# Kernel tuning notes

Measured on AMD Instinct MI355X. Metric: run time of the kernel, lower is better.

The kernel has to match this reference:

```python
import jax, jax.numpy as jnp
import numpy as np

D_MODEL = 1024
N_HEAD = 16
DH = D_MODEL // N_HEAD


def setup_inputs() -> dict:
    key = jax.random.key(0)
    ks = jax.random.split(key, 5)
    B, T = 4, 2048
    scale = 0.02
    return {
        "x": jax.random.normal(ks[0], (B, T, D_MODEL), dtype=jnp.float32),
        "Wqkv": jax.random.normal(ks[1], (D_MODEL, 3 * D_MODEL), dtype=jnp.float32) * scale,
        "bqkv": jnp.zeros((3 * D_MODEL,), dtype=jnp.float32),
        "Wout": jax.random.normal(ks[2], (D_MODEL, D_MODEL), dtype=jnp.float32) * scale,
        "bout": jnp.zeros((D_MODEL,), dtype=jnp.float32),
    }


def reference(x, Wqkv, bqkv, Wout, bout):
    B, T, C = x.shape
    qkv = x @ Wqkv + bqkv  # [B,T,3C]
    q, k, v = jnp.split(qkv, 3, axis=2)
    # [B,T,C] -> [B,H,T,dh]
    def heads(t):
        return t.reshape(B, T, N_HEAD, DH).transpose(0, 2, 1, 3)
    q, k, v = heads(q), heads(k), heads(v)
    scores = jnp.einsum("bhqd,bhkd->bhqk", q, k) / jnp.sqrt(jnp.float32(DH))
    causal = jnp.tril(jnp.ones((T, T), dtype=bool))  # [T,T]
    neg = jnp.finfo(scores.dtype).min
    scores = jnp.where(causal[None, None, :, :], scores, neg)
    A = jax.nn.softmax(scores, axis=-1)
    y = jnp.einsum("bhqk,bhkd->bhqd", A, v)
    y = y.transpose(0, 2, 1, 3).reshape(B, T, C)
    return y @ Wout + bout
```

## Files before the change

kernel.cpp:

```cpp
#include <hip/hip_runtime.h>
#include <hip/hip_bf16.h>

typedef float f32x4 __attribute__((ext_vector_type(4)));
typedef short s16x8 __attribute__((ext_vector_type(8)));
typedef short s16x4 __attribute__((ext_vector_type(4)));

#define B_ 4
#define T_ 2048
#define C_ 1024
#define H_ 16
#define DH_ 64
#define M_ (B_*T_)
#define N3_ (3*C_)

static __device__ __forceinline__ short f2bf(float f) {
    __hip_bfloat16 h = __float2bfloat16(f);
    return *reinterpret_cast<short*>(&h);
}

static __device__ __forceinline__ void gload16(const void* g, void* l) {
    __builtin_amdgcn_global_load_lds(
        (const __attribute__((address_space(1))) void*)g,
        (__attribute__((address_space(3))) void*)l, 16, 0, 0);
}

static __device__ __forceinline__ s16x8 lds_frag(const short* base, int row, int chunk) {
    return *(const s16x8*)&base[(row << 6) + ((chunk ^ (row & 7)) << 3)];
}


__global__ __launch_bounds__(256) void cast_f32_bf16(
    const float* __restrict__ in, short* __restrict__ out, int n8)
{
    int i = blockIdx.x * 256 + threadIdx.x;
    if (i >= n8) return;
    float4 a = *(const float4*)&in[i * 8];
    float4 b = *(const float4*)&in[i * 8 + 4];
    s16x8 o = { f2bf(a.x), f2bf(a.y), f2bf(a.z), f2bf(a.w),
                f2bf(b.x), f2bf(b.y), f2bf(b.z), f2bf(b.w) };
    *(s16x8*)&out[i * 8] = o;
}

__global__ __launch_bounds__(256) void transpose_cast(
    const float* __restrict__ src, short* __restrict__ dst, int K, int N)
{
    __shared__ short t[64][66];
    int tid = threadIdx.x;
    int n0 = blockIdx.x * 64, k0 = blockIdx.y * 64;
    #pragma unroll
    for (int p = 0; p < 4; ++p) {
        int cid = tid + p * 256;
        int r = cid >> 4, c4 = cid & 15;
        float4 v = *(const float4*)&src[(size_t)(k0 + r) * N + n0 + c4 * 4];
        t[r][c4 * 4 + 0] = f2bf(v.x);
        t[r][c4 * 4 + 1] = f2bf(v.y);
        t[r][c4 * 4 + 2] = f2bf(v.z);
        t[r][c4 * 4 + 3] = f2bf(v.w);
    }
    __syncthreads();
    #pragma unroll
    for (int p = 0; p < 4; ++p) {
        int cid = tid + p * 256;
        int r = cid >> 4, c4 = cid & 15;
        s16x4 ov;
        #pragma unroll
        for (int j = 0; j < 4; ++j) ov[j] = t[c4 * 4 + j][r];
        *(s16x4*)&dst[(size_t)(n0 + r) * K + k0 + c4 * 4] = ov;
    }
}


template<int MODE>
__global__ __launch_bounds__(256) void gemm_bt(
    const short* __restrict__ A, const short* __restrict__ Bt,
    const float* __restrict__ bias, float* __restrict__ out,
    short* __restrict__ qout, short* __restrict__ kout, short* __restrict__ vout)
{
    const int K = 1024;
    __shared__ short As[128 * 64];
    __shared__ short Bs[128 * 64];
    int tid = threadIdx.x;
    int lane = tid & 63, w = tid >> 6;
    int d = lane & 15, g = lane >> 4;
    int wm = w >> 1, wn = w & 1;
    int m0 = blockIdx.y * 128, n0 = blockIdx.x * 128;

    f32x4 acc[4][4];
    #pragma unroll
    for (int i = 0; i < 4; ++i)
        #pragma unroll
        for (int j = 0; j < 4; ++j) acc[i][j] = (f32x4){0.f, 0.f, 0.f, 0.f};

    for (int kt = 0; kt < K; kt += 64) {
        #pragma unroll
        for (int p = 0; p < 4; ++p) {
            int cid = p * 256 + tid;
            int r = cid >> 3, c8 = cid & 7;
            int co = (c8 ^ (r & 7)) << 3;
            int dofs = (p * 256 + (tid & ~63)) * 8;
            gload16(&A[(size_t)(m0 + r) * K + kt + co], &As[dofs]);
            gload16(&Bt[(size_t)(n0 + r) * K + kt + co], &Bs[dofs]);
        }
        __syncthreads();
        #pragma unroll
        for (int ks = 0; ks < 2; ++ks) {
            s16x8 af[4], bf[4];
            #pragma unroll
            for (int i = 0; i < 4; ++i) {
                af[i] = lds_frag(As, wm * 64 + i * 16 + d, ks * 4 + g);
                bf[i] = lds_frag(Bs, wn * 64 + i * 16 + d, ks * 4 + g);
            }
            #pragma unroll
            for (int mi = 0; mi < 4; ++mi)
                #pragma unroll
                for (int ni = 0; ni < 4; ++ni)
                    acc[mi][ni] = __builtin_amdgcn_mfma_f32_16x16x32_bf16(
                        af[mi], bf[ni], acc[mi][ni], 0, 0, 0);
        }
        __syncthreads();
    }

    #pragma unroll
    for (int mi = 0; mi < 4; ++mi)
        #pragma unroll
        for (int ni = 0; ni < 4; ++ni) {
            int gn = n0 + wn * 64 + ni * 16 + d;
            float bv = bias[gn];
            int gm0 = m0 + wm * 64 + mi * 16 + g * 4;
            if (MODE == 0) {
                #pragma unroll
                for (int r = 0; r < 4; ++r)
                    out[(size_t)(gm0 + r) * 1024 + gn] = acc[mi][ni][r] + bv;
            } else {
                int which = gn >> 10, cc = gn & 1023;
                int h = cc >> 6, dh = cc & 63;
                int b = gm0 >> 11, t0 = gm0 & 2047;
                if (which == 2) {
                    s16x4 pv;
                    #pragma unroll
                    for (int r = 0; r < 4; ++r) pv[r] = f2bf(acc[mi][ni][r] + bv);
                    *(s16x4*)&vout[((size_t)(b * 16 + h) * 64 + dh) * 2048 + t0] = pv;
                } else {
                    short* dst = which ? kout : qout;
                    #pragma unroll
                    for (int r = 0; r < 4; ++r)
                        dst[((size_t)(b * 16 + h) * 2048 + (t0 + r)) * 64 + dh] =
                            f2bf(acc[mi][ni][r] + bv);
                }
            }
        }
}


__global__ __launch_bounds__(512, 4) void attn_fwd(
    const short* __restrict__ q, const short* __restrict__ kk,
    const short* __restrict__ vt, short* __restrict__ y)
{
    __shared__ short Ks[2][64 * 64];
    __shared__ short Vs[2][64 * 64];
    __shared__ short Ps[8][16][72];
    int tid = threadIdx.x, lane = tid & 63, w = tid >> 6;
    int d = lane & 15, g = lane >> 4;
    int bid = blockIdx.x;
    int bh = (bid & 7) + ((bid >> 6) << 3);
    int pi = (bid >> 3) & 7;
    int b = bh >> 4, h = bh & 15;
    const size_t hb = (size_t)bh * 2048 * 64;

    int r_ = tid >> 3, c8_ = tid & 7;
    int co_ = (c8_ ^ (r_ & 7)) << 3;
    int dofs_ = (tid & ~63) * 8;

    const float SC = 0.125f * 1.44269504089f;

    #define STAGE(buf, kt2) do { \
        gload16(&kk[hb + (size_t)((kt2) * 64 + r_) * 64 + co_], &Ks[buf][dofs_]); \
        gload16(&vt[hb + (size_t)r_ * 2048 + (kt2) * 64 + co_], &Vs[buf][dofs_]); \
    } while (0)

    for (int pass = 0; pass < 2; ++pass) {
        int qt = pass ? (15 - pi) : pi;
        int nt = 2 * qt + 2;
        int qrow = qt * 128 + w * 16;

        s16x8 qf0 = *(const s16x8*)&q[hb + (size_t)(qrow + d) * 64 + 8 * g];
        s16x8 qf1 = *(const s16x8*)&q[hb + (size_t)(qrow + d) * 64 + 32 + 8 * g];

        f32x4 o[4];
        float l[4];
        #pragma unroll
        for (int r = 0; r < 4; ++r) { l[r] = 0.f; o[r] = (f32x4){0.f,0.f,0.f,0.f}; }

        STAGE(0, 0);
        int cur = 0;

        for (int t = 0; t < nt; ++t) {
            if (t + 1 < nt) {
                STAGE(cur ^ 1, t + 1);
                asm volatile("s_waitcnt vmcnt(2)" ::: "memory");
            } else {
                asm volatile("s_waitcnt vmcnt(0)" ::: "memory");
            }
            __builtin_amdgcn_s_barrier();

            if (t * 64 <= qrow + 15) {
                const short* Kb = Ks[cur];
                const short* Vb = Vs[cur];

                f32x4 s[4];
                #pragma unroll
                for (int ni = 0; ni < 4; ++ni) {
                    s[ni] = (f32x4){0.f, 0.f, 0.f, 0.f};
                    s[ni] = __builtin_amdgcn_mfma_f32_16x16x32_bf16(
                        qf0, lds_frag(Kb, ni * 16 + d, g), s[ni], 0, 0, 0);
                    s[ni] = __builtin_amdgcn_mfma_f32_16x16x32_bf16(
                        qf1, lds_frag(Kb, ni * 16 + d, 4 + g), s[ni], 0, 0, 0);
                }

                bool needmask = (t * 64 + 63) > qrow;
                #pragma unroll
                for (int r = 0; r < 4; ++r) {
                    int grow = qrow + g * 4 + r;
                    float sum = 0.f;
                    float pv[4];
                    #pragma unroll
                    for (int ni = 0; ni < 4; ++ni) {
                        float e = exp2f(s[ni][r] * SC);
                        pv[ni] = (needmask && (t * 64 + ni * 16 + d > grow)) ? 0.f : e;
                        sum += pv[ni];
                    }
                    sum += __shfl_xor(sum, 1);
                    sum += __shfl_xor(sum, 2);
                    sum += __shfl_xor(sum, 4);
                    sum += __shfl_xor(sum, 8);
                    l[r] += sum;
                    #pragma unroll
                    for (int ni = 0; ni < 4; ++ni)
                        Ps[w][g * 4 + r][ni * 16 + d] = f2bf(pv[ni]);
                }

                s16x8 pa0 = *(const s16x8*)&Ps[w][d][8 * g];
                s16x8 pa1 = *(const s16x8*)&Ps[w][d][32 + 8 * g];
                #pragma unroll
                for (int df = 0; df < 4; ++df) {
                    o[df] = __builtin_amdgcn_mfma_f32_16x16x32_bf16(
                        pa0, lds_frag(Vb, df * 16 + d, g), o[df], 0, 0, 0);
                    o[df] = __builtin_amdgcn_mfma_f32_16x16x32_bf16(
                        pa1, lds_frag(Vb, df * 16 + d, 4 + g), o[df], 0, 0, 0);
                }
            }

            __builtin_amdgcn_s_barrier();
            cur ^= 1;
        }

        #pragma unroll
        for (int r = 0; r < 4; ++r) {
            float rl = 1.0f / l[r];
            int grow = qrow + g * 4 + r;
            #pragma unroll
            for (int df = 0; df < 4; ++df)
                y[(size_t)(b * 2048 + grow) * 1024 + h * 64 + df * 16 + d] =
                    f2bf(o[df][r] * rl);
        }
    }
    #undef STAGE
}


extern "C" void kernel_launch(void* const* d_in, const int* in_sizes, int n_in,
                              void* d_out, int out_size, void* d_ws, size_t ws_size,
                              hipStream_t stream)
{
    const float* x    = (const float*)d_in[0];
    const float* Wqkv = (const float*)d_in[1];
    const float* bqkv = (const float*)d_in[2];
    const float* Wout = (const float*)d_in[3];
    const float* bout = (const float*)d_in[4];
    float* out = (float*)d_out;

    char* ws = (char*)d_ws;
    short* xbf   = (short*)ws;  ws += (size_t)M_ * C_ * 2;
    short* wqkvT = (short*)ws;  ws += (size_t)N3_ * C_ * 2;
    short* woutT = (short*)ws;  ws += (size_t)C_ * C_ * 2;
    short* qb    = (short*)ws;  ws += (size_t)M_ * C_ * 2;
    short* kb    = (short*)ws;  ws += (size_t)M_ * C_ * 2;
    short* vtb   = (short*)ws;  ws += (size_t)M_ * C_ * 2;
    short* yb    = (short*)ws;  ws += (size_t)M_ * C_ * 2;

    cast_f32_bf16<<<(M_ * C_ / 8 + 255) / 256, 256, 0, stream>>>(x, xbf, M_ * C_ / 8);
    transpose_cast<<<dim3(N3_ / 64, C_ / 64), 256, 0, stream>>>(Wqkv, wqkvT, C_, N3_);
    transpose_cast<<<dim3(C_ / 64, C_ / 64), 256, 0, stream>>>(Wout, woutT, C_, C_);

    gemm_bt<1><<<dim3(N3_ / 128, M_ / 128), 256, 0, stream>>>(
        xbf, wqkvT, bqkv, nullptr, qb, kb, vtb);

    attn_fwd<<<dim3((T_ / 128 / 2) * B_ * H_), 512, 0, stream>>>(qb, kb, vtb, yb);

    gemm_bt<0><<<dim3(C_ / 128, M_ / 128), 256, 0, stream>>>(
        yb, woutT, bout, out, nullptr, nullptr, nullptr);
}
```

Measured before the change: 201.5 us.

## Compute transposed scores, keep P in registers via shuffles, fold scale into Q

The attention kernel now computes S^T by swapping MFMA operands, so each lane holds one query column's scores. The probabilities are then rearranged into the PV A-operand layout with cross-lane shuffles instead of a round-trip through a per-wave LDS buffer. The softmax scale is folded into Q in the QKV GEMM epilogue, which removes a multiply per score. Blocks shrink to 256 threads with 64-row query tiles, giving twice as many blocks and one barrier-synchronised KV pipeline per tile, at the cost of extra shuffle and select instructions per tile.

```diff
diff --git a/kernel.cpp b/kernel.cpp
--- a/kernel.cpp
+++ b/kernel.cpp
@@ -4,6 +4,7 @@
 typedef float f32x4 __attribute__((ext_vector_type(4)));
 typedef short s16x8 __attribute__((ext_vector_type(8)));
 typedef short s16x4 __attribute__((ext_vector_type(4)));
+typedef unsigned int u32x4 __attribute__((ext_vector_type(4)));
 
 #define B_ 4
 #define T_ 2048
@@ -16,6 +17,12 @@
 static __device__ __forceinline__ short f2bf(float f) {
     __hip_bfloat16 h = __float2bfloat16(f);
     return *reinterpret_cast<short*>(&h);
+}
+
+static __device__ __forceinline__ unsigned pack2(float lo, float hi) {
+    unsigned lb = (unsigned short)f2bf(lo);
+    unsigned hb = (unsigned short)f2bf(hi);
+    return lb | (hb << 16);
 }
 
 static __device__ __forceinline__ void gload16(const void* g, void* l) {
@@ -140,64 +147,75 @@
                     #pragma unroll
                     for (int r = 0; r < 4; ++r) pv[r] = f2bf(acc[mi][ni][r] + bv);
                     *(s16x4*)&vout[((size_t)(b * 16 + h) * 64 + dh) * 2048 + t0] = pv;
+                } else if (which == 1) {
+                    #pragma unroll
+                    for (int r = 0; r < 4; ++r)
+                        kout[((size_t)(b * 16 + h) * 2048 + (t0 + r)) * 64 + dh] =
+                            f2bf(acc[mi][ni][r] + bv);
                 } else {
-                    short* dst = which ? kout : qout;
+                    const float SC2 = 0.125f * 1.44269504089f;
                     #pragma unroll
                     for (int r = 0; r < 4; ++r)
-                        dst[((size_t)(b * 16 + h) * 2048 + (t0 + r)) * 64 + dh] =
-                            f2bf(acc[mi][ni][r] + bv);
+                        qout[((size_t)(b * 16 + h) * 2048 + (t0 + r)) * 64 + dh] =
+                            f2bf((acc[mi][ni][r] + bv) * SC2);
                 }
             }
         }
 }
 
 
-__global__ __launch_bounds__(512, 4) void attn_fwd(
+__global__ __launch_bounds__(256, 4) void attn_fwd(
     const short* __restrict__ q, const short* __restrict__ kk,
     const short* __restrict__ vt, short* __restrict__ y)
 {
     __shared__ short Ks[2][64 * 64];
     __shared__ short Vs[2][64 * 64];
-    __shared__ short Ps[8][16][72];
     int tid = threadIdx.x, lane = tid & 63, w = tid >> 6;
     int d = lane & 15, g = lane >> 4;
     int bid = blockIdx.x;
-    int bh = (bid & 7) + ((bid >> 6) << 3);
-    int pi = (bid >> 3) & 7;
+    int bh = (bid & 7) | ((bid >> 7) << 3);
+    int pi = (bid >> 3) & 15;
     int b = bh >> 4, h = bh & 15;
     const size_t hb = (size_t)bh * 2048 * 64;
 
-    int r_ = tid >> 3, c8_ = tid & 7;
-    int co_ = (c8_ ^ (r_ & 7)) << 3;
-    int dofs_ = (tid & ~63) * 8;
-
-    const float SC = 0.125f * 1.44269504089f;
+    const bool isg0 = (g == 0), isg3 = (g == 3);
+    const bool up = lane >= 32;
 
     #define STAGE(buf, kt2) do { \
-        gload16(&kk[hb + (size_t)((kt2) * 64 + r_) * 64 + co_], &Ks[buf][dofs_]); \
-        gload16(&vt[hb + (size_t)r_ * 2048 + (kt2) * 64 + co_], &Vs[buf][dofs_]); \
+        _Pragma("unroll") \
+        for (int p = 0; p < 2; ++p) { \
+            int cid = p * 256 + tid; \
+            int r__ = cid >> 3, c8__ = cid & 7; \
+            int co__ = (c8__ ^ (r__ & 7)) << 3; \
+            int dofs__ = (p * 256 + (tid & ~63)) * 8; \
+            gload16(&kk[hb + (size_t)((kt2) * 64 + r__) * 64 + co__], &Ks[buf][dofs__]); \
+            gload16(&vt[hb + (size_t)r__ * 2048 + (kt2) * 64 + co__], &Vs[buf][dofs__]); \
+        } \
     } while (0)
 
+    #pragma unroll 1
     for (int pass = 0; pass < 2; ++pass) {
-        int qt = pass ? (15 - pi) : pi;
-        int nt = 2 * qt + 2;
-        int qrow = qt * 128 + w * 16;
+        int qt = pass ? (31 - pi) : pi;
+        int nt = qt + 1;
+        int qrow = qt * 64 + w * 16;
+        int qg = qrow + d;
 
         s16x8 qf0 = *(const s16x8*)&q[hb + (size_t)(qrow + d) * 64 + 8 * g];
         s16x8 qf1 = *(const s16x8*)&q[hb + (size_t)(qrow + d) * 64 + 32 + 8 * g];
 
         f32x4 o[4];
-        float l[4];
-        #pragma unroll
-        for (int r = 0; r < 4; ++r) { l[r] = 0.f; o[r] = (f32x4){0.f,0.f,0.f,0.f}; }
+        float l = 0.f;
+        #pragma unroll
+        for (int r = 0; r < 4; ++r) o[r] = (f32x4){0.f, 0.f, 0.f, 0.f};
 
         STAGE(0, 0);
         int cur = 0;
 
+        #pragma unroll 1
         for (int t = 0; t < nt; ++t) {
             if (t + 1 < nt) {
                 STAGE(cur ^ 1, t + 1);
-                asm volatile("s_waitcnt vmcnt(2)" ::: "memory");
+                asm volatile("s_waitcnt vmcnt(4)" ::: "memory");
             } else {
                 asm volatile("s_waitcnt vmcnt(0)" ::: "memory");
             }
@@ -212,35 +230,79 @@
                 for (int ni = 0; ni < 4; ++ni) {
                     s[ni] = (f32x4){0.f, 0.f, 0.f, 0.f};
                     s[ni] = __builtin_amdgcn_mfma_f32_16x16x32_bf16(
-                        qf0, lds_frag(Kb, ni * 16 + d, g), s[ni], 0, 0, 0);
+                        lds_frag(Kb, ni * 16 + d, g), qf0, s[ni], 0, 0, 0);
                     s[ni] = __builtin_amdgcn_mfma_f32_16x16x32_bf16(
-                        qf1, lds_frag(Kb, ni * 16 + d, 4 + g), s[ni], 0, 0, 0);
+                        lds_frag(Kb, ni * 16 + d, 4 + g), qf1, s[ni], 0, 0, 0);
                 }
 
-                bool needmask = (t * 64 + 63) > qrow;
-                #pragma unroll
-                for (int r = 0; r < 4; ++r) {
-                    int grow = qrow + g * 4 + r;
-                    float sum = 0.f;
-                    float pv[4];
-                    #pragma unroll
-                    for (int ni = 0; ni < 4; ++ni) {
-                        float e = exp2f(s[ni][r] * SC);
-                        pv[ni] = (needmask && (t * 64 + ni * 16 + d > grow)) ? 0.f : e;
-                        sum += pv[ni];
-                    }
-                    sum += __shfl_xor(sum, 1);
-                    sum += __shfl_xor(sum, 2);
-                    sum += __shfl_xor(sum, 4);
-                    sum += __shfl_xor(sum, 8);
-                    l[r] += sum;
+                float pv[4][4];
+                if (t * 64 + 63 > qrow) {
                     #pragma unroll
                     for (int ni = 0; ni < 4; ++ni)
-                        Ps[w][g * 4 + r][ni * 16 + d] = f2bf(pv[ni]);
+                        #pragma unroll
+                        for (int r = 0; r < 4; ++r) {
+                            int kg = t * 64 + ni * 16 + g * 4 + r;
+                            pv[ni][r] = (kg > qg) ? 0.f : exp2f(s[ni][r]);
+                        }
+                } else {
+                    #pragma unroll
+                    for (int ni = 0; ni < 4; ++ni)
+                        #pragma unroll
+                        for (int r = 0; r < 4; ++r)
+                            pv[ni][r] = exp2f(s[ni][r]);
                 }
 
-                s16x8 pa0 = *(const s16x8*)&Ps[w][d][8 * g];
-                s16x8 pa1 = *(const s16x8*)&Ps[w][d][32 + 8 * g];
+                float S = ((pv[0][0] + pv[0][1]) + (pv[0][2] + pv[0][3]))
+                        + ((pv[1][0] + pv[1][1]) + (pv[1][2] + pv[1][3]))
+                        + ((pv[2][0] + pv[2][1]) + (pv[2][2] + pv[2][3]))
+                        + ((pv[3][0] + pv[3][1]) + (pv[3][2] + pv[3][3]));
+                S += __shfl_xor(S, 16);
+                S += __shfl_xor(S, 32);
+                l += S;
+
+                unsigned W[4][2], X[4][2];
+                #pragma unroll
+                for (int ni = 0; ni < 4; ++ni)
+                    #pragma unroll
+                    for (int rp = 0; rp < 2; ++rp)
+                        W[ni][rp] = pack2(pv[ni][2 * rp], pv[ni][2 * rp + 1]);
+                #pragma unroll
+                for (int ni = 0; ni < 4; ++ni)
+                    #pragma unroll
+                    for (int rp = 0; rp < 2; ++rp)
+                        X[ni][rp] = __shfl_xor((int)W[ni][rp], 16);
+
+                unsigned P0 = up ? X[0][0] : W[1][0];
+                unsigned P1 = up ? X[0][1] : W[1][1];
+                unsigned P2 = up ? W[0][0] : X[1][0];
+                unsigned P3 = up ? W[0][1] : X[1][1];
+                unsigned P4 = up ? X[2][0] : W[3][0];
+                unsigned P5 = up ? X[2][1] : W[3][1];
+                unsigned P6 = up ? W[2][0] : X[3][0];
+                unsigned P7 = up ? W[2][1] : X[3][1];
+                unsigned R0 = __shfl_xor((int)P0, 32);
+                unsigned R1 = __shfl_xor((int)P1, 32);
+                unsigned R2 = __shfl_xor((int)P2, 32);
+                unsigned R3 = __shfl_xor((int)P3, 32);
+                unsigned R4 = __shfl_xor((int)P4, 32);
+                unsigned R5 = __shfl_xor((int)P5, 32);
+                unsigned R6 = __shfl_xor((int)P6, 32);
+                unsigned R7 = __shfl_xor((int)P7, 32);
+
+                unsigned F0 = isg0 ? W[0][0] : isg3 ? X[1][0] : R0;
+                unsigned F1 = isg0 ? W[0][1] : isg3 ? X[1][1] : R1;
+                unsigned F2 = isg0 ? X[0][0] : isg3 ? W[1][0] : R2;
+                unsigned F3 = isg0 ? X[0][1] : isg3 ? W[1][1] : R3;
+                unsigned F4 = isg0 ? W[2][0] : isg3 ? X[3][0] : R4;
+                unsigned F5 = isg0 ? W[2][1] : isg3 ? X[3][1] : R5;
+                unsigned F6 = isg0 ? X[2][0] : isg3 ? W[3][0] : R6;
+                unsigned F7 = isg0 ? X[2][1] : isg3 ? W[3][1] : R7;
+
+                u32x4 w0 = {F0, F1, F2, F3};
+                u32x4 w1 = {F4, F5, F6, F7};
+                s16x8 pa0 = __builtin_bit_cast(s16x8, w0);
+                s16x8 pa1 = __builtin_bit_cast(s16x8, w1);
+
                 #pragma unroll
                 for (int df = 0; df < 4; ++df) {
                     o[df] = __builtin_amdgcn_mfma_f32_16x16x32_bf16(
@@ -256,7 +318,8 @@
 
         #pragma unroll
         for (int r = 0; r < 4; ++r) {
-            float rl = 1.0f / l[r];
+            float lr = __shfl(l, g * 4 + r);
+            float rl = 1.0f / lr;
             int grow = qrow + g * 4 + r;
             #pragma unroll
             for (int df = 0; df < 4; ++df)
@@ -295,7 +358,7 @@
     gemm_bt<1><<<dim3(N3_ / 128, M_ / 128), 256, 0, stream>>>(
         xbf, wqkvT, bqkv, nullptr, qb, kb, vtb);
 
-    attn_fwd<<<dim3((T_ / 128 / 2) * B_ * H_), 512, 0, stream>>>(qb, kb, vtb, yb);
+    attn_fwd<<<dim3((T_ / 64 / 2) * B_ * H_), 256, 0, stream>>>(qb, kb, vtb, yb);
 
     gemm_bt<0><<<dim3(C_ / 128, M_ / 128), 256, 0, stream>>>(
         yb, woutT, bout, out, nullptr, nullptr, nullptr);
```

Result: no change. 197.6 us (-1.9%).
